# Optimization experiments

Measured on AMD Instinct MI355X. Metric: run time of the kernel, lower is better.

Reference implementation:

```python
import jax, jax.numpy as jnp
import numpy as np

B, S, D = 2, 2048, 1024
H = 16
HD = D // H  # 64
SCALE = HD ** -0.5


def setup_inputs() -> dict:
    key = jax.random.key(0)
    ks = jax.random.split(key, 9)
    init = lambda k, shape: jax.random.normal(k, shape, dtype=jnp.float32) * (1.0 / np.sqrt(shape[-1]))
    return {
        "x": jax.random.normal(ks[0], (B, S, D), dtype=jnp.float32),
        "wq": init(ks[1], (D, D)), "bq": jnp.zeros((D,), jnp.float32),
        "wk": init(ks[2], (D, D)), "bk": jnp.zeros((D,), jnp.float32),
        "wv": init(ks[3], (D, D)), "bv": jnp.zeros((D,), jnp.float32),
        "wo": init(ks[4], (D, D)), "bo": jnp.zeros((D,), jnp.float32),
    }


def reference(x, wq, bq, wk, bk, wv, bv, wo, bo):
    b, s, d = x.shape
    # projections -> [b, h, s, hd]
    q = (x @ wq + bq).reshape(b, s, H, HD).transpose(0, 2, 1, 3)
    k = (x @ wk + bk).reshape(b, s, H, HD).transpose(0, 2, 1, 3)
    v = (x @ wv + bv).reshape(b, s, H, HD).transpose(0, 2, 1, 3)
    # full causal attention (chunked loop in original computes exactly this)
    scores = jnp.einsum("bhqd,bhkd->bhqk", q, k) * SCALE
    causal = jnp.tril(jnp.ones((s, s), dtype=bool))
    scores = jnp.where(causal, scores, -jnp.inf)
    weights = jax.nn.softmax(scores, axis=-1)
    out = jnp.einsum("bhqk,bhkd->bhqd", weights, v)
    out = out.transpose(0, 2, 1, 3).reshape(b, s, d)
    return out @ wo + bo
```

## Files before the change

### kernel.cpp

```cpp
#include <hip/hip_runtime.h>
#include <hip/hip_bf16.h>
#include <cstdint>

#define B_  2
#define S_  2048
#define D_  1024
#define H_  16
#define HD_ 64
#define M_  (B_ * S_)
static constexpr float SC_LOG2E = 0.125f * 1.44269504088896f;

typedef __bf16 bf16x8 __attribute__((ext_vector_type(8)));
typedef __bf16 bf16x4 __attribute__((ext_vector_type(4)));
typedef float  f32x4  __attribute__((ext_vector_type(4)));

__device__ __forceinline__ unsigned short f2b(float f) {
  union { float f; unsigned u; } x; x.f = f;
  unsigned r = x.u + 0x7FFF + ((x.u >> 16) & 1);
  return (unsigned short)(r >> 16);
}

__device__ __forceinline__ void gl_lds16(const unsigned short* g, unsigned short* l) {
  __builtin_amdgcn_global_load_lds((const __attribute__((address_space(1))) void*)g,
                                   (__attribute__((address_space(3))) void*)l, 16, 0, 0);
}

__device__ __forceinline__ void bar_lgkm() {
  asm volatile("s_waitcnt lgkmcnt(0)\n\ts_barrier" ::: "memory");
}
__device__ __forceinline__ void bar_vm2() {
  asm volatile("s_waitcnt vmcnt(2) lgkmcnt(0)\n\ts_barrier" ::: "memory");
}
__device__ __forceinline__ void bar_vm0() {
  asm volatile("s_waitcnt vmcnt(0) lgkmcnt(0)\n\ts_barrier" ::: "memory");
}

__global__ void cvt_all_kernel(const float* __restrict__ x,
                               const float* __restrict__ w0, const float* __restrict__ w1,
                               const float* __restrict__ w2, const float* __restrict__ w3,
                               unsigned short* __restrict__ xb,
                               unsigned short* __restrict__ o0, unsigned short* __restrict__ o1,
                               unsigned short* __restrict__ o2, unsigned short* __restrict__ o3) {
  int tx = threadIdx.x, ty = threadIdx.y;
  if (blockIdx.z == 4) {
    int tid = ty * 32 + tx;
    int base = ((int)blockIdx.y * 32 + (int)blockIdx.x) * 1024 + tid;
    const float4* xf = (const float4*)x;
    ushort4* ob = (ushort4*)xb;
#pragma unroll
    for (int j = 0; j < 4; j++) {
      float4 v = xf[base + j * 256];
      ushort4 r;
      r.x = f2b(v.x); r.y = f2b(v.y); r.z = f2b(v.z); r.w = f2b(v.w);
      ob[base + j * 256] = r;
    }
    return;
  }
  const float* w = blockIdx.z == 0 ? w0 : blockIdx.z == 1 ? w1 : blockIdx.z == 2 ? w2 : w3;
  unsigned short* o = blockIdx.z == 0 ? o0 : blockIdx.z == 1 ? o1 : blockIdx.z == 2 ? o2 : o3;
  __shared__ float t[32][33];
  int x0 = blockIdx.x * 32, y0 = blockIdx.y * 32;
#pragma unroll
  for (int j = 0; j < 4; j++)
    t[ty + j * 8][tx] = w[(size_t)(y0 + ty + j * 8) * D_ + x0 + tx];
  __syncthreads();
#pragma unroll
  for (int j = 0; j < 4; j++)
    o[(size_t)(x0 + ty + j * 8) * D_ + y0 + tx] = f2b(t[tx][ty + j * 8]);
}

__global__ __launch_bounds__(512) void qkv_gemm_kernel(
    const unsigned short* __restrict__ xb,
    const unsigned short* __restrict__ wqt, const unsigned short* __restrict__ wkt,
    const unsigned short* __restrict__ wvt,
    const float* __restrict__ bq, const float* __restrict__ bk, const float* __restrict__ bv,
    unsigned short* __restrict__ qo, unsigned short* __restrict__ ko, unsigned short* __restrict__ vo) {
  const unsigned short* wt = blockIdx.z == 0 ? wqt : blockIdx.z == 1 ? wkt : wvt;
  const float* bias        = blockIdx.z == 0 ? bq  : blockIdx.z == 1 ? bk  : bv;
  unsigned short* out      = blockIdx.z == 0 ? qo  : blockIdx.z == 1 ? ko  : vo;
  const float scl = blockIdx.z == 0 ? SC_LOG2E : 1.0f;

  __shared__ __align__(16) unsigned short smem[6 * 4096];
  const int tid = threadIdx.x;
  const int lane = tid & 63, wid = tid >> 6;
  const int wm = wid & 1, wn = wid >> 1;
  const int m0 = blockIdx.x * 128, n0 = blockIdx.y * 128;
  const int l15 = lane & 15, q4 = lane >> 4;
  const int srow = tid >> 2, skc = (tid & 3) * 8;

  f32x4 zero = {0.f, 0.f, 0.f, 0.f};
  f32x4 acc[4][2];
#pragma unroll
  for (int mt = 0; mt < 4; mt++)
#pragma unroll
    for (int nt = 0; nt < 2; nt++) acc[mt][nt] = zero;

  const unsigned short* ap = xb + (size_t)(m0 + srow) * D_ + skc;
  const unsigned short* bp = wt + (size_t)(n0 + srow) * D_ + skc;
  gl_lds16(ap,      smem + tid * 8);
  gl_lds16(bp,      smem + 12288 + tid * 8);
  gl_lds16(ap + 32, smem + 4096 + tid * 8);
  gl_lds16(bp + 32, smem + 12288 + 4096 + tid * 8);

  int bc = 0;
  for (int it = 0; it < 32; it++) {
    if (it < 31) bar_vm2(); else bar_vm0();
    if (it + 2 < 32) {
      int bn_ = bc < 1 ? bc + 2 : bc - 1;
      gl_lds16(ap + (it + 2) * 32, smem + bn_ * 4096 + tid * 8);
      gl_lds16(bp + (it + 2) * 32, smem + 12288 + bn_ * 4096 + tid * 8);
    }
    const unsigned short* Ab = smem + bc * 4096;
    const unsigned short* Bb = smem + 12288 + bc * 4096;
    bf16x8 af[4], bfv[2];
#pragma unroll
    for (int mt = 0; mt < 4; mt++) af[mt]  = *(const bf16x8*)(Ab + (wm * 64 + mt * 16 + l15) * 32 + q4 * 8);
#pragma unroll
    for (int nt = 0; nt < 2; nt++) bfv[nt] = *(const bf16x8*)(Bb + (wn * 32 + nt * 16 + l15) * 32 + q4 * 8);
#pragma unroll
    for (int mt = 0; mt < 4; mt++)
#pragma unroll
      for (int nt = 0; nt < 2; nt++)
        acc[mt][nt] = __builtin_amdgcn_mfma_f32_16x16x32_bf16(af[mt], bfv[nt], acc[mt][nt], 0, 0, 0);
    bc = bc == 2 ? 0 : bc + 1;
  }

  if (blockIdx.z < 2) {
#pragma unroll
    for (int nt = 0; nt < 2; nt++) {
      int n = n0 + wn * 32 + nt * 16 + l15;
      float bn = bias[n];
      int h = n >> 6, hd = n & 63;
#pragma unroll
      for (int mt = 0; mt < 4; mt++) {
#pragma unroll
        for (int r = 0; r < 4; r++) {
          int m = m0 + wm * 64 + mt * 16 + q4 * 4 + r;
          int b = m >> 11, s = m & (S_ - 1);
          out[(((size_t)(b * H_ + h)) * S_ + s) * HD_ + hd] = f2b((acc[mt][nt][r] + bn) * scl);
        }
      }
    }
  } else {
    unsigned short* buf = smem;
#pragma unroll
    for (int p = 0; p < 2; p++) {
      __syncthreads();
      if ((wn >> 1) == p) {
#pragma unroll
        for (int nt = 0; nt < 2; nt++) {
          int np = (wn & 1) * 32 + nt * 16 + l15;
          float bn = bias[n0 + p * 64 + np];
#pragma unroll
          for (int mt = 0; mt < 4; mt++) {
            f32x4 vb = acc[mt][nt];
            vb[0] += bn; vb[1] += bn; vb[2] += bn; vb[3] += bn;
            bf16x4 pk = __builtin_convertvector(vb, bf16x4);
            *(bf16x4*)(&buf[np * 136 + wm * 64 + mt * 16 + q4 * 4]) = pk;
          }
        }
      }
      __syncthreads();
#pragma unroll
      for (int i = 0; i < 2; i++) {
        int ci = tid + i * 512;
        int np = ci >> 4, c = ci & 15;
        int n = n0 + p * 64 + np;
        int h = n >> 6, hd = n & 63;
        int m = m0 + c * 8;
        int b = m >> 11, s = m & (S_ - 1);
        *(uint4*)(out + (((size_t)(b * H_ + h)) * HD_ + hd) * S_ + s) = *(const uint4*)(buf + np * 136 + c * 8);
      }
    }
  }
}

__global__ __launch_bounds__(512, 4) void attn_kernel(
    const unsigned short* __restrict__ Q, const unsigned short* __restrict__ K,
    const unsigned short* __restrict__ Vt_g, unsigned short* __restrict__ O) {
  const int id = blockIdx.x;
  const int u = id >> 8, v = id & 255;
  const int bh = v & 31;
  const int t = v >> 5;
  const int qi = u ? (15 - t) : t;
  const int b = bh >> 4, h = bh & 15;
  const unsigned short* Qh = Q    + (size_t)bh * S_ * HD_;
  const unsigned short* Kh = K    + (size_t)bh * S_ * HD_;
  const unsigned short* Vh = Vt_g + (size_t)bh * HD_ * S_;

  __shared__ __align__(16) unsigned short Ks[2][64 * 64];
  __shared__ __align__(16) unsigned short Vt[2][64 * 64];
  __shared__ __align__(16) unsigned short Ps[8][16 * 72];

  const int tid = threadIdx.x, lane = tid & 63, w = tid >> 6;
  const int l15 = lane & 15, q4 = lane >> 4;
  const int kx = (l15 & 7) << 3;
  const int kcA = (q4 * 8) ^ kx, kcB = (q4 * 8 + 32) ^ kx;
  const int vc0 = (q4 * 8) ^ kx, vc1 = (32 + q4 * 8) ^ kx;
  unsigned short* Pw = &Ps[w][0];

  const int srow = tid >> 3;
  const int scolS = (((tid & 7) ^ (srow & 7)) * 8);
  const unsigned short* kg = Kh + (size_t)srow * HD_ + (tid & 7) * 8;
  const unsigned short* vg = Vh + (size_t)srow * S_  + (tid & 7) * 8;

  const int q0 = qi * 128;
  const int nkt = 2 * qi + 2;
  const int qlo = q0 + w * 16;
  const int qmax = qlo + 15;
  const int qrow = qlo + l15;

  const unsigned short* qp = Qh + (size_t)qrow * HD_ + q4 * 8;
  bf16x8 bq0 = *(const bf16x8*)(qp);
  bf16x8 bq1 = *(const bf16x8*)(qp + 32);

  float m_i = -1e30f, l_i = 0.f;
  f32x4 zero = {0.f, 0.f, 0.f, 0.f};
  f32x4 o_acc[4];
#pragma unroll
  for (int t4 = 0; t4 < 4; t4++) o_acc[t4] = zero;

  uint4 kp = *(const uint4*)(kg);
  uint4 vp = *(const uint4*)(vg);

  for (int kt = 0; kt < nkt; kt++) {
    const int k0 = kt * 64;
    unsigned short* Kb = Ks[kt & 1];
    unsigned short* Vb = Vt[kt & 1];
    *(uint4*)(Kb + srow * 64 + scolS) = kp;
    *(uint4*)(Vb + srow * 64 + scolS) = vp;
    bar_lgkm();
    if (kt + 1 < nkt) {
      kp = *(const uint4*)(kg + (size_t)(kt + 1) * 64 * HD_);
      vp = *(const uint4*)(vg + (kt + 1) * 64);
    }

    if (k0 <= qmax) {
      f32x4 sc[4];
#pragma unroll
      for (int nt = 0; nt < 4; nt++) sc[nt] = zero;
      __builtin_amdgcn_s_setprio(1);
#pragma unroll
      for (int nt = 0; nt < 4; nt++) {
        bf16x8 ak0 = *(const bf16x8*)(Kb + (nt * 16 + l15) * 64 + kcA);
        bf16x8 ak1 = *(const bf16x8*)(Kb + (nt * 16 + l15) * 64 + kcB);
        sc[nt] = __builtin_amdgcn_mfma_f32_16x16x32_bf16(ak0, bq0, sc[nt], 0, 0, 0);
        sc[nt] = __builtin_amdgcn_mfma_f32_16x16x32_bf16(ak1, bq1, sc[nt], 0, 0, 0);
      }
      __builtin_amdgcn_s_setprio(0);

      if ((k0 + 63) > qlo) {
#pragma unroll
        for (int nt = 0; nt < 4; nt++)
#pragma unroll
          for (int r = 0; r < 4; r++) {
            int key = k0 + nt * 16 + q4 * 4 + r;
            if (key > qrow) sc[nt][r] = -1e30f;
          }
      }

      float am[4];
#pragma unroll
      for (int nt = 0; nt < 4; nt++)
        am[nt] = fmaxf(fmaxf(sc[nt][0], sc[nt][1]), fmaxf(sc[nt][2], sc[nt][3]));
      am[0] = fmaxf(am[0], am[2]); am[1] = fmaxf(am[1], am[3]);
      float mx = fmaxf(am[0], am[1]);
      mx = fmaxf(mx, __shfl_xor(mx, 16));
      mx = fmaxf(mx, __shfl_xor(mx, 32));
      mx = fmaxf(mx, m_i);

      if (!__all(mx - m_i <= 10.0f)) {
        float alpha = __builtin_amdgcn_exp2f(m_i - mx);
        m_i = mx;
        l_i *= alpha;
#pragma unroll
        for (int r = 0; r < 4; r++) {
          float ar = __shfl(alpha, q4 * 4 + r);
          o_acc[0][r] *= ar; o_acc[1][r] *= ar; o_acc[2][r] *= ar; o_acc[3][r] *= ar;
        }
      }

      float sm[4];
#pragma unroll
      for (int nt = 0; nt < 4; nt++) {
        f32x4 pv;
#pragma unroll
        for (int r = 0; r < 4; r++) pv[r] = __builtin_amdgcn_exp2f(sc[nt][r] - m_i);
        sc[nt] = pv;
        sm[nt] = (pv[0] + pv[1]) + (pv[2] + pv[3]);
      }
      float rs = (sm[0] + sm[2]) + (sm[1] + sm[3]);
      rs += __shfl_xor(rs, 16);
      rs += __shfl_xor(rs, 32);
      l_i += rs;

#pragma unroll
      for (int nt = 0; nt < 4; nt++) {
        bf16x4 pk = __builtin_convertvector(sc[nt], bf16x4);
        *(bf16x4*)(Pw + l15 * 72 + nt * 16 + q4 * 4) = pk;
      }
      __threadfence_block();
      bf16x8 ap0 = *(const bf16x8*)(Pw + l15 * 72 + q4 * 8);
      bf16x8 ap1 = *(const bf16x8*)(Pw + l15 * 72 + 32 + q4 * 8);
      __builtin_amdgcn_s_setprio(1);
#pragma unroll
      for (int nt2 = 0; nt2 < 4; nt2++) {
        bf16x8 bv0 = *(const bf16x8*)(Vb + (nt2 * 16 + l15) * 64 + vc0);
        o_acc[nt2] = __builtin_amdgcn_mfma_f32_16x16x32_bf16(ap0, bv0, o_acc[nt2], 0, 0, 0);
      }
#pragma unroll
      for (int nt2 = 0; nt2 < 4; nt2++) {
        bf16x8 bv1 = *(const bf16x8*)(Vb + (nt2 * 16 + l15) * 64 + vc1);
        o_acc[nt2] = __builtin_amdgcn_mfma_f32_16x16x32_bf16(ap1, bv1, o_acc[nt2], 0, 0, 0);
      }
      __builtin_amdgcn_s_setprio(0);
    }
  }

#pragma unroll
  for (int r = 0; r < 4; r++) {
    float lr = __shfl(l_i, q4 * 4 + r);
    float inv = 1.0f / lr;
    int s_ = q0 + w * 16 + q4 * 4 + r;
#pragma unroll
    for (int nt2 = 0; nt2 < 4; nt2++)
      O[((size_t)(b * S_ + s_)) * D_ + h * HD_ + nt2 * 16 + l15] = f2b(o_acc[nt2][r] * inv);
  }
}

__global__ __launch_bounds__(512) void out_gemm_kernel(
    const unsigned short* __restrict__ ab, const unsigned short* __restrict__ wot,
    const float* __restrict__ bo, float* __restrict__ out) {
  __shared__ __align__(16) unsigned short smem[6 * 4096];
  const int tid = threadIdx.x;
  const int lane = tid & 63, wid = tid >> 6;
  const int wm = wid & 1, wn = wid >> 1;
  const int m0 = blockIdx.x * 128, n0 = blockIdx.y * 128;
  const int l15 = lane & 15, q4 = lane >> 4;
  const int srow = tid >> 2, skc = (tid & 3) * 8;

  f32x4 zero = {0.f, 0.f, 0.f, 0.f};
  f32x4 acc[4][2];
#pragma unroll
  for (int mt = 0; mt < 4; mt++)
#pragma unroll
    for (int nt = 0; nt < 2; nt++) acc[mt][nt] = zero;

  const unsigned short* ap = ab  + (size_t)(m0 + srow) * D_ + skc;
  const unsigned short* bp = wot + (size_t)(n0 + srow) * D_ + skc;
  gl_lds16(ap,      smem + tid * 8);
  gl_lds16(bp,      smem + 12288 + tid * 8);
  gl_lds16(ap + 32, smem + 4096 + tid * 8);
  gl_lds16(bp + 32, smem + 12288 + 4096 + tid * 8);

  int bc = 0;
  for (int it = 0; it < 32; it++) {
    if (it < 31) bar_vm2(); else bar_vm0();
    if (it + 2 < 32) {
      int bn_ = bc < 1 ? bc + 2 : bc - 1;
      gl_lds16(ap + (it + 2) * 32, smem + bn_ * 4096 + tid * 8);
      gl_lds16(bp + (it + 2) * 32, smem + 12288 + bn_ * 4096 + tid * 8);
    }
    const unsigned short* Ab = smem + bc * 4096;
    const unsigned short* Bb = smem + 12288 + bc * 4096;
    bf16x8 af[4], bfv[2];
#pragma unroll
    for (int mt = 0; mt < 4; mt++) af[mt]  = *(const bf16x8*)(Ab + (wm * 64 + mt * 16 + l15) * 32 + q4 * 8);
#pragma unroll
    for (int nt = 0; nt < 2; nt++) bfv[nt] = *(const bf16x8*)(Bb + (wn * 32 + nt * 16 + l15) * 32 + q4 * 8);
#pragma unroll
    for (int mt = 0; mt < 4; mt++)
#pragma unroll
      for (int nt = 0; nt < 2; nt++)
        acc[mt][nt] = __builtin_amdgcn_mfma_f32_16x16x32_bf16(af[mt], bfv[nt], acc[mt][nt], 0, 0, 0);
    bc = bc == 2 ? 0 : bc + 1;
  }

#pragma unroll
  for (int nt = 0; nt < 2; nt++) {
    int n = n0 + wn * 32 + nt * 16 + l15;
    float bn = bo[n];
#pragma unroll
    for (int mt = 0; mt < 4; mt++) {
#pragma unroll
      for (int r = 0; r < 4; r++) {
        int m = m0 + wm * 64 + mt * 16 + q4 * 4 + r;
        out[(size_t)m * D_ + n] = acc[mt][nt][r] + bn;
      }
    }
  }
}

extern "C" void kernel_launch(void* const* d_in, const int* in_sizes, int n_in,
                              void* d_out, int out_size, void* d_ws, size_t ws_size,
                              hipStream_t stream) {
  const float* x  = (const float*)d_in[0];
  const float* wq = (const float*)d_in[1];
  const float* bq = (const float*)d_in[2];
  const float* wk = (const float*)d_in[3];
  const float* bk = (const float*)d_in[4];
  const float* wv = (const float*)d_in[5];
  const float* bv = (const float*)d_in[6];
  const float* wo = (const float*)d_in[7];
  const float* bo = (const float*)d_in[8];
  float* out = (float*)d_out;

  char* ws = (char*)d_ws;
  unsigned short* xb  = (unsigned short*)(ws);
  unsigned short* wqt = (unsigned short*)(ws + (8u  << 20));
  unsigned short* wkt = (unsigned short*)(ws + (10u << 20));
  unsigned short* wvt = (unsigned short*)(ws + (12u << 20));
  unsigned short* wot = (unsigned short*)(ws + (14u << 20));
  unsigned short* qb  = (unsigned short*)(ws + (16u << 20));
  unsigned short* kb  = (unsigned short*)(ws + (24u << 20));
  unsigned short* vtg = (unsigned short*)(ws + (32u << 20));
  unsigned short* ab  = xb;

  cvt_all_kernel<<<dim3(32, 32, 5), dim3(32, 8), 0, stream>>>(x, wq, wk, wv, wo, xb, wqt, wkt, wvt, wot);
  qkv_gemm_kernel<<<dim3(32, 8, 3), dim3(512), 0, stream>>>(xb, wqt, wkt, wvt, bq, bk, bv, qb, kb, vtg);
  attn_kernel<<<dim3(512), dim3(512), 0, stream>>>(qb, kb, vtg, ab);
  out_gemm_kernel<<<dim3(32, 8), dim3(512), 0, stream>>>(ab, wot, bo, out);
}
```

Baseline: 181.7 us.

## Split heavy causal query tiles across two blocks with a merge kernel

Heavy (late) causal query tiles are now processed by two blocks, each taking alternate key tiles, and they write unnormalized partial outputs plus running max and sum to a float workspace. A new merge kernel rescales and combines the two partials and writes the bf16 attention output. Light tiles keep a single pass. The goal is better load balance and more blocks in flight (launch bounds raised to 6 waves per SIMD hint). The cost is an extra launch, partial-result global traffic, and possible register pressure from the tighter launch bound.

```diff
diff --git a/kernel.cpp b/kernel.cpp
--- a/kernel.cpp
+++ b/kernel.cpp
@@ -13,6 +13,8 @@
 typedef __bf16 bf16x8 __attribute__((ext_vector_type(8)));
 typedef __bf16 bf16x4 __attribute__((ext_vector_type(4)));
 typedef float  f32x4  __attribute__((ext_vector_type(4)));
+
+#define PPLANE (256 * 2 * 512)
 
 __device__ __forceinline__ unsigned short f2b(float f) {
   union { float f; unsigned u; } x; x.f = f;
@@ -175,14 +177,16 @@
   }
 }
 
-__global__ __launch_bounds__(512, 4) void attn_kernel(
+__global__ __launch_bounds__(512, 6) void attn_kernel(
     const unsigned short* __restrict__ Q, const unsigned short* __restrict__ K,
-    const unsigned short* __restrict__ Vt_g, unsigned short* __restrict__ O) {
+    const unsigned short* __restrict__ Vt_g, unsigned short* __restrict__ O,
+    float* __restrict__ part) {
   const int id = blockIdx.x;
-  const int u = id >> 8, v = id & 255;
-  const int bh = v & 31;
-  const int t = v >> 5;
-  const int qi = u ? (15 - t) : t;
+  const int g = id & 255, r = id >> 8;
+  const int bh = g & 31, j = g >> 5;
+  const bool heavy = (r < 2);
+  const int qi = heavy ? (15 - j) : j;
+  const int split = heavy ? r : 0;
   const int b = bh >> 4, h = bh & 15;
   const unsigned short* Qh = Q    + (size_t)bh * S_ * HD_;
   const unsigned short* Kh = K    + (size_t)bh * S_ * HD_;
@@ -205,7 +209,8 @@
   const unsigned short* vg = Vh + (size_t)srow * S_  + (tid & 7) * 8;
 
   const int q0 = qi * 128;
-  const int nkt = 2 * qi + 2;
+  const int nst = heavy ? (qi + 1) : (2 * qi + 2);
+  const int kstep = heavy ? 2 : 1;
   const int qlo = q0 + w * 16;
   const int qmax = qlo + 15;
   const int qrow = qlo + l15;
@@ -220,19 +225,21 @@
 #pragma unroll
   for (int t4 = 0; t4 < 4; t4++) o_acc[t4] = zero;
 
-  uint4 kp = *(const uint4*)(kg);
-  uint4 vp = *(const uint4*)(vg);
-
-  for (int kt = 0; kt < nkt; kt++) {
+  uint4 kp = *(const uint4*)(kg + (size_t)split * 64 * HD_);
+  uint4 vp = *(const uint4*)(vg + split * 64);
+
+  for (int s = 0; s < nst; s++) {
+    const int kt = kstep * s + split;
     const int k0 = kt * 64;
-    unsigned short* Kb = Ks[kt & 1];
-    unsigned short* Vb = Vt[kt & 1];
+    unsigned short* Kb = Ks[s & 1];
+    unsigned short* Vb = Vt[s & 1];
     *(uint4*)(Kb + srow * 64 + scolS) = kp;
     *(uint4*)(Vb + srow * 64 + scolS) = vp;
     bar_lgkm();
-    if (kt + 1 < nkt) {
-      kp = *(const uint4*)(kg + (size_t)(kt + 1) * 64 * HD_);
-      vp = *(const uint4*)(vg + (kt + 1) * 64);
+    if (s + 1 < nst) {
+      const int ktn = kt + kstep;
+      kp = *(const uint4*)(kg + (size_t)ktn * 64 * HD_);
+      vp = *(const uint4*)(vg + ktn * 64);
     }
 
     if (k0 <= qmax) {
@@ -253,9 +260,9 @@
 #pragma unroll
         for (int nt = 0; nt < 4; nt++)
 #pragma unroll
-          for (int r = 0; r < 4; r++) {
-            int key = k0 + nt * 16 + q4 * 4 + r;
-            if (key > qrow) sc[nt][r] = -1e30f;
+          for (int r2 = 0; r2 < 4; r2++) {
+            int key = k0 + nt * 16 + q4 * 4 + r2;
+            if (key > qrow) sc[nt][r2] = -1e30f;
           }
       }
 
@@ -274,9 +281,9 @@
         m_i = mx;
         l_i *= alpha;
 #pragma unroll
-        for (int r = 0; r < 4; r++) {
-          float ar = __shfl(alpha, q4 * 4 + r);
-          o_acc[0][r] *= ar; o_acc[1][r] *= ar; o_acc[2][r] *= ar; o_acc[3][r] *= ar;
+        for (int r2 = 0; r2 < 4; r2++) {
+          float ar = __shfl(alpha, q4 * 4 + r2);
+          o_acc[0][r2] *= ar; o_acc[1][r2] *= ar; o_acc[2][r2] *= ar; o_acc[3][r2] *= ar;
         }
       }
 
@@ -285,7 +292,7 @@
       for (int nt = 0; nt < 4; nt++) {
         f32x4 pv;
 #pragma unroll
-        for (int r = 0; r < 4; r++) pv[r] = __builtin_amdgcn_exp2f(sc[nt][r] - m_i);
+        for (int r2 = 0; r2 < 4; r2++) pv[r2] = __builtin_amdgcn_exp2f(sc[nt][r2] - m_i);
         sc[nt] = pv;
         sm[nt] = (pv[0] + pv[1]) + (pv[2] + pv[3]);
       }
@@ -317,14 +324,62 @@
     }
   }
 
-#pragma unroll
-  for (int r = 0; r < 4; r++) {
-    float lr = __shfl(l_i, q4 * 4 + r);
-    float inv = 1.0f / lr;
-    int s_ = q0 + w * 16 + q4 * 4 + r;
+  if (heavy) {
+    float* P = part + ((size_t)(g * 2 + split) * 512 + tid);
 #pragma unroll
     for (int nt2 = 0; nt2 < 4; nt2++)
-      O[((size_t)(b * S_ + s_)) * D_ + h * HD_ + nt2 * 16 + l15] = f2b(o_acc[nt2][r] * inv);
+#pragma unroll
+      for (int r2 = 0; r2 < 4; r2++) P[(size_t)(nt2 * 4 + r2) * PPLANE] = o_acc[nt2][r2];
+    P[(size_t)16 * PPLANE] = m_i;
+    P[(size_t)17 * PPLANE] = l_i;
+  } else {
+#pragma unroll
+    for (int r2 = 0; r2 < 4; r2++) {
+      float lr = __shfl(l_i, q4 * 4 + r2);
+      float inv = 1.0f / lr;
+      int s_ = q0 + w * 16 + q4 * 4 + r2;
+#pragma unroll
+      for (int nt2 = 0; nt2 < 4; nt2++)
+        O[((size_t)(b * S_ + s_)) * D_ + h * HD_ + nt2 * 16 + l15] = f2b(o_acc[nt2][r2] * inv);
+    }
+  }
+}
+
+__global__ __launch_bounds__(512) void attn_merge_kernel(
+    const float* __restrict__ part, unsigned short* __restrict__ O) {
+  const int g = blockIdx.x;
+  const int bh = g & 31, j = g >> 5;
+  const int qi = 15 - j;
+  const int b = bh >> 4, h = bh & 15;
+  const int tid = threadIdx.x, lane = tid & 63, w = tid >> 6;
+  const int l15 = lane & 15, q4 = lane >> 4;
+
+  const float* P0 = part + ((size_t)(g * 2 + 0) * 512 + tid);
+  const float* P1 = part + ((size_t)(g * 2 + 1) * 512 + tid);
+  float o0[16], o1[16];
+#pragma unroll
+  for (int i = 0; i < 16; i++) {
+    o0[i] = P0[(size_t)i * PPLANE];
+    o1[i] = P1[(size_t)i * PPLANE];
+  }
+  float m0 = P0[(size_t)16 * PPLANE], l0 = P0[(size_t)17 * PPLANE];
+  float m1 = P1[(size_t)16 * PPLANE], l1 = P1[(size_t)17 * PPLANE];
+  float m  = fmaxf(m0, m1);
+  float a0 = __builtin_amdgcn_exp2f(m0 - m);
+  float a1 = __builtin_amdgcn_exp2f(m1 - m);
+  float l  = l0 * a0 + l1 * a1;
+
+  const int q0 = qi * 128;
+#pragma unroll
+  for (int r2 = 0; r2 < 4; r2++) {
+    float ar0 = __shfl(a0, q4 * 4 + r2);
+    float ar1 = __shfl(a1, q4 * 4 + r2);
+    float inv = 1.0f / __shfl(l, q4 * 4 + r2);
+    int s_ = q0 + w * 16 + q4 * 4 + r2;
+#pragma unroll
+    for (int nt2 = 0; nt2 < 4; nt2++)
+      O[((size_t)(b * S_ + s_)) * D_ + h * HD_ + nt2 * 16 + l15] =
+          f2b((o0[nt2 * 4 + r2] * ar0 + o1[nt2 * 4 + r2] * ar1) * inv);
   }
 }
 
@@ -414,10 +469,12 @@
   unsigned short* qb  = (unsigned short*)(ws + (16u << 20));
   unsigned short* kb  = (unsigned short*)(ws + (24u << 20));
   unsigned short* vtg = (unsigned short*)(ws + (32u << 20));
+  float*          prt = (float*)(ws + (40u << 20));
   unsigned short* ab  = xb;
 
   cvt_all_kernel<<<dim3(32, 32, 5), dim3(32, 8), 0, stream>>>(x, wq, wk, wv, wo, xb, wqt, wkt, wvt, wot);
   qkv_gemm_kernel<<<dim3(32, 8, 3), dim3(512), 0, stream>>>(xb, wqt, wkt, wvt, bq, bk, bv, qb, kb, vtg);
-  attn_kernel<<<dim3(512), dim3(512), 0, stream>>>(qb, kb, vtg, ab);
+  attn_kernel<<<dim3(768), dim3(512), 0, stream>>>(qb, kb, vtg, ab, prt);
+  attn_merge_kernel<<<dim3(256), dim3(512), 0, stream>>>(prt, ab);
   out_gemm_kernel<<<dim3(32, 8), dim3(512), 0, stream>>>(ab, wot, bo, out);
 }
```

Result: no change. 181.5 us (-0.1%).
